# Kernel optimization log

Hardware: AMD Instinct MI355X
Metric: run time of the kernel (lower is better)

The kernel has to match this reference:

```python
import jax, jax.numpy as jnp
import numpy as np

N_NODES = 1024
H = 256        # hidden_dim
HEADS = 4
EPS = 1e-5     # torch LayerNorm default


def _ln(x, g, b):
    m = x.mean(-1, keepdims=True)
    v = ((x - m) ** 2).mean(-1, keepdims=True)
    return (x - m) / jnp.sqrt(v + EPS) * g + b


def setup_inputs() -> dict:
    key = jax.random.key(0)
    ks = jax.random.split(key, 24)
    B, L = 16, 64
    P = N_NODES * (N_NODES - 1) // 2
    D0 = L + 7  # latent_dim + 7 stats
    s = 0.02
    f32 = jnp.float32
    d = {}
    d['x'] = jax.random.normal(ks[0], (B, L), f32)
    d['stats'] = jax.random.normal(ks[1], (B, 7), f32)
    d['u'] = jax.random.uniform(ks[2], (B, P, 2), f32)  # uniform noise -> gumbel
    d['ln0_g'] = jnp.ones((D0,), f32); d['ln0_b'] = jnp.zeros((D0,), f32)
    # residual block 1 (in D0 -> H, has projection)
    d['rb1_ln_g'] = jnp.ones((D0,), f32); d['rb1_ln_b'] = jnp.zeros((D0,), f32)
    d['rb1_w1'] = jax.random.normal(ks[3], (H, D0), f32) * s; d['rb1_b1'] = jnp.zeros((H,), f32)
    d['rb1_w2'] = jax.random.normal(ks[4], (H, H), f32) * s;  d['rb1_b2'] = jnp.zeros((H,), f32)
    d['rb1_wp'] = jax.random.normal(ks[5], (H, D0), f32) * s; d['rb1_bp'] = jnp.zeros((H,), f32)
    # residual block 2 (H -> H, no projection)
    d['rb2_ln_g'] = jnp.ones((H,), f32); d['rb2_ln_b'] = jnp.zeros((H,), f32)
    d['rb2_w1'] = jax.random.normal(ks[6], (H, H), f32) * s; d['rb2_b1'] = jnp.zeros((H,), f32)
    d['rb2_w2'] = jax.random.normal(ks[7], (H, H), f32) * s; d['rb2_b2'] = jnp.zeros((H,), f32)
    # GraphAttention: LN + MHA(in_proj, out_proj) + output Linear
    d['att_ln_g'] = jnp.ones((H,), f32); d['att_ln_b'] = jnp.zeros((H,), f32)
    d['att_win'] = jax.random.normal(ks[8], (3 * H, H), f32) * s; d['att_bin'] = jnp.zeros((3 * H,), f32)
    d['att_wout'] = jax.random.normal(ks[9], (H, H), f32) * s;    d['att_bout'] = jnp.zeros((H,), f32)
    d['out_w'] = jax.random.normal(ks[10], (H, H), f32) * s;      d['out_b'] = jnp.zeros((H,), f32)
    # final edge-logit layer over concat([h_i, h_j]) -> 2
    d['fin_w'] = jax.random.normal(ks[11], (2, 2 * H), f32) * s;  d['fin_b'] = jnp.zeros((2,), f32)
    d['temp'] = jnp.ones((1,), f32)
    return d


def reference(x, stats, u, ln0_g, ln0_b,
              rb1_ln_g, rb1_ln_b, rb1_w1, rb1_b1, rb1_w2, rb1_b2, rb1_wp, rb1_bp,
              rb2_ln_g, rb2_ln_b, rb2_w1, rb2_b1, rb2_w2, rb2_b2,
              att_ln_g, att_ln_b, att_win, att_bin, att_wout, att_bout,
              out_w, out_b, fin_w, fin_b, temp):
    B = x.shape[0]
    z = jnp.concatenate([x, stats], axis=-1)          # [B, D0]
    z = _ln(z, ln0_g, ln0_b)
    h = jnp.broadcast_to(z[:, None, :], (B, N_NODES, z.shape[-1]))  # [B, N, D0]
    # residual block 1 (dropout in eval mode = identity)
    t = _ln(h, rb1_ln_g, rb1_ln_b)
    t = jax.nn.gelu(t @ rb1_w1.T + rb1_b1, approximate=False)
    t = t @ rb1_w2.T + rb1_b2
    h = t + (h @ rb1_wp.T + rb1_bp)                   # [B, N, H]
    # residual block 2
    t = _ln(h, rb2_ln_g, rb2_ln_b)
    t = jax.nn.gelu(t @ rb2_w1.T + rb2_b1, approximate=False)
    t = t @ rb2_w2.T + rb2_b2
    h = t + h
    # GraphAttention: LN -> self MHA -> output linear
    a = _ln(h, att_ln_g, att_ln_b)
    qkv = a @ att_win.T + att_bin                      # [B, N, 3H]
    q, k, v = jnp.split(qkv, 3, axis=-1)
    dh = H // HEADS
    def heads(t):
        return t.reshape(B, N_NODES, HEADS, dh).transpose(0, 2, 1, 3)
    q, k, v = heads(q), heads(k), heads(v)
    scores = jnp.einsum('bhqd,bhkd->bhqk', q, k) * np.float32(1.0 / np.sqrt(dh))
    att = jax.nn.softmax(scores, axis=-1)
    o = jnp.einsum('bhqk,bhkd->bhqd', att, v).transpose(0, 2, 1, 3).reshape(B, N_NODES, H)
    o = o @ att_wout.T + att_bout
    h = o @ out_w.T + out_b                            # [B, N, H]
    # pairwise edge logits: Linear(cat(h_i, h_j)) == h_i @ W_a^T + h_j @ W_b^T + b
    la = h @ fin_w[:, :H].T                            # [B, N, 2]
    lb = h @ fin_w[:, H:].T                            # [B, N, 2]
    iu, ju = jnp.triu_indices(N_NODES, k=1)
    logits = la[:, iu] + lb[:, ju] + fin_b             # [B, P, 2]
    # gumbel-softmax (hard, straight-through), tau = |temperature|
    tau = jnp.abs(temp)[0]
    g = -jnp.log(-jnp.log(u + 1e-10) + 1e-10)
    y_soft = jax.nn.softmax((logits + g) / tau, axis=-1)
    y_hard = jax.nn.one_hot(jnp.argmax(y_soft, axis=-1), 2, dtype=y_soft.dtype)
    y = y_hard + y_soft - jax.lax.stop_gradient(y_soft)
    e = y[..., 0]                                      # [B, P]
    adj = jnp.zeros((B, N_NODES, N_NODES), e.dtype).at[:, iu, ju].set(e)
    return adj + adj.transpose(0, 2, 1)
```

## Files before the change

kernel.cpp:

```cpp
#include <hip/hip_runtime.h>
#include <math.h>


#define NN    1024
#define HD    256
#define DIN0  71
#define NPAIR 523776
#define TILE  64
#define NT    16

__device__ __forceinline__ double blk_reduce(double v, double* red) {
  const int t = threadIdx.x;
  red[t] = v;
  __syncthreads();
  #pragma unroll
  for (int s = 128; s > 0; s >>= 1) {
    if (t < s) red[t] += red[t + s];
    __syncthreads();
  }
  double r = red[0];
  __syncthreads();
  return r;
}

__device__ __forceinline__ void ln_to(const double* src, double* dst, int D,
                                      const float* __restrict__ gam,
                                      const float* __restrict__ bet,
                                      double* red) {
  const int tid = threadIdx.x;
  double v = (tid < D) ? src[tid] : 0.0;
  double m = blk_reduce(v, red) / (double)D;
  double d = (tid < D) ? (src[tid] - m) : 0.0;
  double var = blk_reduce(d * d, red) / (double)D;
  double inv = 1.0 / sqrt(var + (double)1e-5f);
  if (tid < D) dst[tid] = d * inv * (double)gam[tid] + (double)bet[tid];
  __syncthreads();
}

__device__ __forceinline__ double dotw(const double* src, int Din,
                                       const float* __restrict__ W, int row) {
  const float* wr = W + (size_t)row * Din;
  double acc = 0.0;
  if ((Din & 3) == 0) {
    const float4* w4 = reinterpret_cast<const float4*>(wr);
    const int n4 = Din >> 2;
    #pragma unroll 4
    for (int i = 0; i < n4; ++i) {
      float4 w = w4[i];
      acc += src[4*i+0] * (double)w.x;
      acc += src[4*i+1] * (double)w.y;
      acc += src[4*i+2] * (double)w.z;
      acc += src[4*i+3] * (double)w.w;
    }
  } else {
    for (int i = 0; i < Din; ++i) acc += src[i] * (double)wr[i];
  }
  return acc;
}

__device__ __forceinline__ double gelu_exact(double x) {
  return 0.5 * x * (1.0 + erf(x * 0.70710678118654752440));
}

__global__ __launch_bounds__(256)
void head_kernel(const float* __restrict__ x, const float* __restrict__ stats,
                 const float* __restrict__ ln0_g, const float* __restrict__ ln0_b,
                 const float* __restrict__ rb1_ln_g, const float* __restrict__ rb1_ln_b,
                 const float* __restrict__ rb1_w1, const float* __restrict__ rb1_b1,
                 const float* __restrict__ rb1_w2, const float* __restrict__ rb1_b2,
                 const float* __restrict__ rb1_wp, const float* __restrict__ rb1_bp,
                 const float* __restrict__ rb2_ln_g, const float* __restrict__ rb2_ln_b,
                 const float* __restrict__ rb2_w1, const float* __restrict__ rb2_b1,
                 const float* __restrict__ rb2_w2, const float* __restrict__ rb2_b2,
                 const float* __restrict__ att_ln_g, const float* __restrict__ att_ln_b,
                 const float* __restrict__ att_win, const float* __restrict__ att_bin,
                 const float* __restrict__ att_wout, const float* __restrict__ att_bout,
                 const float* __restrict__ out_w, const float* __restrict__ out_b,
                 const float* __restrict__ fin_w, const float* __restrict__ fin_b,
                 double* __restrict__ c_out) {
  __shared__ double h[HD], t[HD], g[HD], red[256];
  const int tid = threadIdx.x;
  const int b = blockIdx.x;

  if (tid < DIN0)
    h[tid] = (tid < 64) ? (double)x[b * 64 + tid] : (double)stats[b * 7 + tid - 64];
  __syncthreads();

  ln_to(h, h, DIN0, ln0_g, ln0_b, red);

  ln_to(h, t, DIN0, rb1_ln_g, rb1_ln_b, red);
  g[tid] = gelu_exact(dotw(t, DIN0, rb1_w1, tid) + (double)rb1_b1[tid]);
  __syncthreads();
  {
    double t2 = dotw(g, HD, rb1_w2, tid) + (double)rb1_b2[tid];
    double pr = dotw(h, DIN0, rb1_wp, tid) + (double)rb1_bp[tid];
    __syncthreads();
    h[tid] = t2 + pr;
  }
  __syncthreads();

  ln_to(h, t, HD, rb2_ln_g, rb2_ln_b, red);
  g[tid] = gelu_exact(dotw(t, HD, rb2_w1, tid) + (double)rb2_b1[tid]);
  __syncthreads();
  {
    double t2 = dotw(g, HD, rb2_w2, tid) + (double)rb2_b2[tid];
    h[tid] = h[tid] + t2;
  }
  __syncthreads();

  ln_to(h, t, HD, att_ln_g, att_ln_b, red);
  g[tid] = dotw(t, HD, att_win + 2 * HD * HD, tid) + (double)att_bin[2 * HD + tid];
  __syncthreads();
  t[tid] = dotw(g, HD, att_wout, tid) + (double)att_bout[tid];
  __syncthreads();
  double hj = dotw(t, HD, out_w, tid) + (double)out_b[tid];

  double v0 = hj * (double)fin_w[tid]          + hj * (double)fin_w[HD + tid];
  double v1 = hj * (double)fin_w[2 * HD + tid] + hj * (double)fin_w[3 * HD + tid];
  double c0 = blk_reduce(v0, red) + (double)fin_b[0];
  double c1 = blk_reduce(v1, red) + (double)fin_b[1];
  if (tid == 0) {
    c_out[2 * b + 0] = c0;
    c_out[2 * b + 1] = c1;
  }
}

__global__ __launch_bounds__(256)
void adj_tile_kernel(const float* __restrict__ u, const double* __restrict__ c,
                     float* __restrict__ out) {
  __shared__ float tile[TILE][TILE + 1];
  const int b = blockIdx.y;
  int k = blockIdx.x;
  int ti = 0;
  while (k >= NT - ti) { k -= NT - ti; ++ti; }
  const int tj = ti + k;
  const bool diag = (ti == tj);

  const int t        = threadIdx.x;
  const int lane_col = (t & 15) << 2;
  const int row_base = t >> 4;
  const double c0 = c[2 * b + 0];
  const double c1 = c[2 * b + 1];
  const float* ub = u + (size_t)b * (2u * NPAIR);
  float* ob = out + ((size_t)b << 20);

  #pragma unroll
  for (int s = 0; s < 4; ++s) {
    const int il = s * 16 + row_base;
    const int i  = ti * TILE + il;
    const int rb = i * (2 * NN - 1 - i) / 2 - i - 1;
    float4 ev4;
    float* ev = &ev4.x;
    #pragma unroll
    for (int q = 0; q < 4; ++q) {
      const int jl = lane_col + q;
      const int j  = tj * TILE + jl;
      float e = 0.0f;
      if (j > i) {
        const int p = rb + j;
        const float2 uu = *reinterpret_cast<const float2*>(ub + 2 * p);
        const float g0 = -logf(-logf(uu.x + 1e-10f) + 1e-10f);
        const float g1 = -logf(-logf(uu.y + 1e-10f) + 1e-10f);
        e = ((c0 + (double)g0) >= (c1 + (double)g1)) ? 1.0f : 0.0f;
      }
      ev[q] = e;
      tile[il][jl] = e;
    }
    if (!diag) {
      *reinterpret_cast<float4*>(ob + (size_t)i * NN + tj * TILE + lane_col) = ev4;
    }
  }
  __syncthreads();

  #pragma unroll
  for (int s = 0; s < 4; ++s) {
    const int rl = s * 16 + row_base;
    if (!diag) {
      float4 v = make_float4(tile[lane_col + 0][rl], tile[lane_col + 1][rl],
                             tile[lane_col + 2][rl], tile[lane_col + 3][rl]);
      *reinterpret_cast<float4*>(ob + (size_t)(tj * TILE + rl) * NN
                                    + ti * TILE + lane_col) = v;
    } else {
      float v[4];
      #pragma unroll
      for (int q = 0; q < 4; ++q) {
        const int jl = lane_col + q;
        v[q] = (jl > rl) ? tile[rl][jl] : ((jl < rl) ? tile[jl][rl] : 0.0f);
      }
      *reinterpret_cast<float4*>(ob + (size_t)(ti * TILE + rl) * NN
                                    + ti * TILE + lane_col)
          = make_float4(v[0], v[1], v[2], v[3]);
    }
  }
}

extern "C" void kernel_launch(void* const* d_in, const int* in_sizes, int n_in,
                              void* d_out, int out_size, void* d_ws, size_t ws_size,
                              hipStream_t stream) {
  const float* x        = (const float*)d_in[0];
  const float* stats    = (const float*)d_in[1];
  const float* u        = (const float*)d_in[2];
  const float* ln0_g    = (const float*)d_in[3];
  const float* ln0_b    = (const float*)d_in[4];
  const float* rb1_ln_g = (const float*)d_in[5];
  const float* rb1_ln_b = (const float*)d_in[6];
  const float* rb1_w1   = (const float*)d_in[7];
  const float* rb1_b1   = (const float*)d_in[8];
  const float* rb1_w2   = (const float*)d_in[9];
  const float* rb1_b2   = (const float*)d_in[10];
  const float* rb1_wp   = (const float*)d_in[11];
  const float* rb1_bp   = (const float*)d_in[12];
  const float* rb2_ln_g = (const float*)d_in[13];
  const float* rb2_ln_b = (const float*)d_in[14];
  const float* rb2_w1   = (const float*)d_in[15];
  const float* rb2_b1   = (const float*)d_in[16];
  const float* rb2_w2   = (const float*)d_in[17];
  const float* rb2_b2   = (const float*)d_in[18];
  const float* att_ln_g = (const float*)d_in[19];
  const float* att_ln_b = (const float*)d_in[20];
  const float* att_win  = (const float*)d_in[21];
  const float* att_bin  = (const float*)d_in[22];
  const float* att_wout = (const float*)d_in[23];
  const float* att_bout = (const float*)d_in[24];
  const float* out_w    = (const float*)d_in[25];
  const float* out_b    = (const float*)d_in[26];
  const float* fin_w    = (const float*)d_in[27];
  const float* fin_b    = (const float*)d_in[28];

  double* c_ws = (double*)d_ws;
  float* out   = (float*)d_out;

  hipLaunchKernelGGL(head_kernel, dim3(16), dim3(256), 0, stream,
                     x, stats, ln0_g, ln0_b,
                     rb1_ln_g, rb1_ln_b, rb1_w1, rb1_b1, rb1_w2, rb1_b2, rb1_wp, rb1_bp,
                     rb2_ln_g, rb2_ln_b, rb2_w1, rb2_b1, rb2_w2, rb2_b2,
                     att_ln_g, att_ln_b, att_win, att_bin, att_wout, att_bout,
                     out_w, out_b, fin_w, fin_b, c_ws);

  hipLaunchKernelGGL(adj_tile_kernel, dim3(NT * (NT + 1) / 2, 16), dim3(256), 0, stream,
                     u, c_ws, out);
}
```

Before: 252.0 us.

## Prefetch weights into cache, use wave-shuffle reductions and split dot accumulators

A separate kernel launches before the head kernel and reads all MLP and attention weight matrices, so they are cache-resident when the 16-block head kernel streams them. Eight blocks per stripe read the same data, apparently so every L2 slice is warmed. The shared-memory tree reduction is replaced by a 64-lane shuffle plus a four-wave combine, which cuts the number of barriers. The float4 dot product now uses four independent double accumulators to shorten the dependency chain. The extra launch and redundant reads add overhead, and the summation order changes slightly.

```diff
diff --git a/kernel.cpp b/kernel.cpp
--- a/kernel.cpp
+++ b/kernel.cpp
@@ -9,18 +9,50 @@
 #define TILE  64
 #define NT    16
 
+__device__ __forceinline__ float pf_sum(const float4* __restrict__ p, int n4,
+                                        int stripe, int tid) {
+  float s = 0.0f;
+  for (int i = stripe * 256 + tid; i < n4; i += 256 * 256) {
+    float4 v = p[i];
+    s += v.x + v.y + v.z + v.w;
+  }
+  return s;
+}
+
+__global__ __launch_bounds__(256)
+void prefetch_kernel(const float* __restrict__ w0, int n0,
+                     const float* __restrict__ w1, int n1,
+                     const float* __restrict__ w2, int n2,
+                     const float* __restrict__ w3, int n3,
+                     const float* __restrict__ w4, int n4_,
+                     const float* __restrict__ w5, int n5,
+                     const float* __restrict__ w6, int n6,
+                     const float* __restrict__ w7, int n7,
+                     const float* __restrict__ w8, int n8,
+                     float* __restrict__ sink) {
+  const int stripe = blockIdx.x >> 3;
+  const int tid = threadIdx.x;
+  float s = 0.0f;
+  s += pf_sum((const float4*)w0, n0 >> 2, stripe, tid);
+  s += pf_sum((const float4*)w1, n1 >> 2, stripe, tid);
+  s += pf_sum((const float4*)w2, n2 >> 2, stripe, tid);
+  s += pf_sum((const float4*)w3, n3 >> 2, stripe, tid);
+  s += pf_sum((const float4*)w4, n4_ >> 2, stripe, tid);
+  s += pf_sum((const float4*)w5, n5 >> 2, stripe, tid);
+  s += pf_sum((const float4*)w6, n6 >> 2, stripe, tid);
+  s += pf_sum((const float4*)w7, n7 >> 2, stripe, tid);
+  s += pf_sum((const float4*)w8, n8 >> 2, stripe, tid);
+  if (s == 123456789.0f) sink[0] = s;
+}
+
 __device__ __forceinline__ double blk_reduce(double v, double* red) {
-  const int t = threadIdx.x;
-  red[t] = v;
-  __syncthreads();
   #pragma unroll
-  for (int s = 128; s > 0; s >>= 1) {
-    if (t < s) red[t] += red[t + s];
-    __syncthreads();
-  }
-  double r = red[0];
-  __syncthreads();
-  return r;
+  for (int m = 32; m > 0; m >>= 1) v += __shfl_xor(v, m, 64);
+  const int wid = threadIdx.x >> 6;
+  __syncthreads();
+  if ((threadIdx.x & 63) == 0) red[wid] = v;
+  __syncthreads();
+  return (red[0] + red[1]) + (red[2] + red[3]);
 }
 
 __device__ __forceinline__ void ln_to(const double* src, double* dst, int D,
@@ -40,21 +72,22 @@
 __device__ __forceinline__ double dotw(const double* src, int Din,
                                        const float* __restrict__ W, int row) {
   const float* wr = W + (size_t)row * Din;
-  double acc = 0.0;
   if ((Din & 3) == 0) {
     const float4* w4 = reinterpret_cast<const float4*>(wr);
     const int n4 = Din >> 2;
+    double a0 = 0.0, a1 = 0.0, a2 = 0.0, a3 = 0.0;
     #pragma unroll 4
     for (int i = 0; i < n4; ++i) {
       float4 w = w4[i];
-      acc += src[4*i+0] * (double)w.x;
-      acc += src[4*i+1] * (double)w.y;
-      acc += src[4*i+2] * (double)w.z;
-      acc += src[4*i+3] * (double)w.w;
-    }
-  } else {
-    for (int i = 0; i < Din; ++i) acc += src[i] * (double)wr[i];
-  }
+      a0 += src[4*i+0] * (double)w.x;
+      a1 += src[4*i+1] * (double)w.y;
+      a2 += src[4*i+2] * (double)w.z;
+      a3 += src[4*i+3] * (double)w.w;
+    }
+    return (a0 + a1) + (a2 + a3);
+  }
+  double acc = 0.0;
+  for (int i = 0; i < Din; ++i) acc += src[i] * (double)wr[i];
   return acc;
 }
 
@@ -78,7 +111,7 @@
                  const float* __restrict__ out_w, const float* __restrict__ out_b,
                  const float* __restrict__ fin_w, const float* __restrict__ fin_b,
                  double* __restrict__ c_out) {
-  __shared__ double h[HD], t[HD], g[HD], red[256];
+  __shared__ double h[HD], t[HD], g[HD], red[8];
   const int tid = threadIdx.x;
   const int b = blockIdx.x;
 
@@ -228,7 +261,20 @@
   const float* fin_b    = (const float*)d_in[28];
 
   double* c_ws = (double*)d_ws;
+  float* sink  = (float*)d_ws + 64;
   float* out   = (float*)d_out;
+
+  hipLaunchKernelGGL(prefetch_kernel, dim3(2048), dim3(256), 0, stream,
+                     rb1_w1, HD * DIN0 - (HD * DIN0 % 4),
+                     rb1_w2, HD * HD,
+                     rb1_wp, HD * DIN0 - (HD * DIN0 % 4),
+                     rb2_w1, HD * HD,
+                     rb2_w2, HD * HD,
+                     att_win + 2 * HD * HD, HD * HD,
+                     att_wout, HD * HD,
+                     out_w, HD * HD,
+                     fin_w, 4 * HD,
+                     sink);
 
   hipLaunchKernelGGL(head_kernel, dim3(16), dim3(256), 0, stream,
                      x, stats, ln0_g, ln0_b,
```

After: 248.0 us. Within noise of the previous version (-1.6%).

## Split head MLP dot products across four threads per row with shuffle reductions

Applied to the files above, without the earlier changes.

The head kernel now runs 1024 threads per block, and each output row's dot product is split across a quad of four threads whose partial sums are combined with xor shuffles. The shared-memory tree block reduction is replaced by a wavefront shuffle reduction followed by a small cross-wave sum. The goal is to shorten the serial, latency-bound per-batch head stage that runs on only 16 blocks. The cost is a larger block and more barriers of 1024 threads, and the head stage may be a small share of total time next to the adjacency kernel.

```diff
diff --git a/kernel.cpp b/kernel.cpp
--- a/kernel.cpp
+++ b/kernel.cpp
@@ -8,19 +8,19 @@
 #define NPAIR 523776
 #define TILE  64
 #define NT    16
+#define HT    1024
 
 __device__ __forceinline__ double blk_reduce(double v, double* red) {
-  const int t = threadIdx.x;
-  red[t] = v;
-  __syncthreads();
-  #pragma unroll
-  for (int s = 128; s > 0; s >>= 1) {
-    if (t < s) red[t] += red[t + s];
-    __syncthreads();
-  }
-  double r = red[0];
-  __syncthreads();
-  return r;
+  #pragma unroll
+  for (int m = 32; m > 0; m >>= 1) v += __shfl_xor(v, m, 64);
+  const int wid = threadIdx.x >> 6;
+  __syncthreads();
+  if ((threadIdx.x & 63) == 0) red[wid] = v;
+  __syncthreads();
+  double s = 0.0;
+  #pragma unroll
+  for (int w = 0; w < HT / 64; ++w) s += red[w];
+  return s;
 }
 
 __device__ __forceinline__ void ln_to(const double* src, double* dst, int D,
@@ -37,32 +37,45 @@
   __syncthreads();
 }
 
-__device__ __forceinline__ double dotw(const double* src, int Din,
-                                       const float* __restrict__ W, int row) {
-  const float* wr = W + (size_t)row * Din;
-  double acc = 0.0;
-  if ((Din & 3) == 0) {
-    const float4* w4 = reinterpret_cast<const float4*>(wr);
-    const int n4 = Din >> 2;
-    #pragma unroll 4
-    for (int i = 0; i < n4; ++i) {
-      float4 w = w4[i];
-      acc += src[4*i+0] * (double)w.x;
-      acc += src[4*i+1] * (double)w.y;
-      acc += src[4*i+2] * (double)w.z;
-      acc += src[4*i+3] * (double)w.w;
-    }
-  } else {
-    for (int i = 0; i < Din; ++i) acc += src[i] * (double)wr[i];
-  }
-  return acc;
+__device__ __forceinline__ double dot4_256(const double* src,
+                                           const float* __restrict__ W,
+                                           int row, int p) {
+  const float4* w4 = reinterpret_cast<const float4*>(W + (size_t)row * 256);
+  double a0 = 0.0, a1 = 0.0, a2 = 0.0, a3 = 0.0;
+  #pragma unroll
+  for (int k = 0; k < 16; ++k) {
+    const int f = p + 4 * k;
+    float4 w = w4[f];
+    const double* s = src + 4 * f;
+    a0 += s[0] * (double)w.x;
+    a1 += s[1] * (double)w.y;
+    a2 += s[2] * (double)w.z;
+    a3 += s[3] * (double)w.w;
+  }
+  return (a0 + a1) + (a2 + a3);
+}
+
+__device__ __forceinline__ double dot4_71(const double* src,
+                                          const float* __restrict__ W,
+                                          int row, int p) {
+  const float* wr = W + (size_t)row * DIN0;
+  double a = 0.0;
+  #pragma unroll
+  for (int i = p; i < DIN0; i += 4) a += src[i] * (double)wr[i];
+  return a;
+}
+
+__device__ __forceinline__ double quad_sum(double v) {
+  v += __shfl_xor(v, 1, 64);
+  v += __shfl_xor(v, 2, 64);
+  return v;
 }
 
 __device__ __forceinline__ double gelu_exact(double x) {
   return 0.5 * x * (1.0 + erf(x * 0.70710678118654752440));
 }
 
-__global__ __launch_bounds__(256)
+__global__ __launch_bounds__(HT)
 void head_kernel(const float* __restrict__ x, const float* __restrict__ stats,
                  const float* __restrict__ ln0_g, const float* __restrict__ ln0_b,
                  const float* __restrict__ rb1_ln_g, const float* __restrict__ rb1_ln_b,
@@ -78,9 +91,11 @@
                  const float* __restrict__ out_w, const float* __restrict__ out_b,
                  const float* __restrict__ fin_w, const float* __restrict__ fin_b,
                  double* __restrict__ c_out) {
-  __shared__ double h[HD], t[HD], g[HD], red[256];
+  __shared__ double h[HD], t[HD], g[HD], red[HT / 64];
   const int tid = threadIdx.x;
   const int b = blockIdx.x;
+  const int r = tid >> 2;
+  const int p = tid & 3;
 
   if (tid < DIN0)
     h[tid] = (tid < 64) ? (double)x[b * 64 + tid] : (double)stats[b * 7 + tid - 64];
@@ -89,34 +104,54 @@
   ln_to(h, h, DIN0, ln0_g, ln0_b, red);
 
   ln_to(h, t, DIN0, rb1_ln_g, rb1_ln_b, red);
-  g[tid] = gelu_exact(dotw(t, DIN0, rb1_w1, tid) + (double)rb1_b1[tid]);
-  __syncthreads();
-  {
-    double t2 = dotw(g, HD, rb1_w2, tid) + (double)rb1_b2[tid];
-    double pr = dotw(h, DIN0, rb1_wp, tid) + (double)rb1_bp[tid];
+  {
+    double d = quad_sum(dot4_71(t, rb1_w1, r, p));
+    if (p == 0) g[r] = gelu_exact(d + (double)rb1_b1[r]);
+  }
+  __syncthreads();
+  {
+    double d2 = quad_sum(dot4_256(g, rb1_w2, r, p));
+    double dp = quad_sum(dot4_71(h, rb1_wp, r, p));
     __syncthreads();
-    h[tid] = t2 + pr;
+    if (p == 0) h[r] = (d2 + (double)rb1_b2[r]) + (dp + (double)rb1_bp[r]);
   }
   __syncthreads();
 
   ln_to(h, t, HD, rb2_ln_g, rb2_ln_b, red);
-  g[tid] = gelu_exact(dotw(t, HD, rb2_w1, tid) + (double)rb2_b1[tid]);
-  __syncthreads();
-  {
-    double t2 = dotw(g, HD, rb2_w2, tid) + (double)rb2_b2[tid];
-    h[tid] = h[tid] + t2;
+  {
+    double d = quad_sum(dot4_256(t, rb2_w1, r, p));
+    if (p == 0) g[r] = gelu_exact(d + (double)rb2_b1[r]);
+  }
+  __syncthreads();
+  {
+    double d = quad_sum(dot4_256(g, rb2_w2, r, p));
+    if (p == 0) h[r] = h[r] + (d + (double)rb2_b2[r]);
   }
   __syncthreads();
 
   ln_to(h, t, HD, att_ln_g, att_ln_b, red);
-  g[tid] = dotw(t, HD, att_win + 2 * HD * HD, tid) + (double)att_bin[2 * HD + tid];
-  __syncthreads();
-  t[tid] = dotw(g, HD, att_wout, tid) + (double)att_bout[tid];
-  __syncthreads();
-  double hj = dotw(t, HD, out_w, tid) + (double)out_b[tid];
-
-  double v0 = hj * (double)fin_w[tid]          + hj * (double)fin_w[HD + tid];
-  double v1 = hj * (double)fin_w[2 * HD + tid] + hj * (double)fin_w[3 * HD + tid];
+  {
+    double d = quad_sum(dot4_256(t, att_win + 2 * HD * HD, r, p));
+    if (p == 0) g[r] = d + (double)att_bin[2 * HD + r];
+  }
+  __syncthreads();
+  {
+    double d = quad_sum(dot4_256(g, att_wout, r, p));
+    if (p == 0) t[r] = d + (double)att_bout[r];
+  }
+  __syncthreads();
+  {
+    double d = quad_sum(dot4_256(t, out_w, r, p));
+    if (p == 0) g[r] = d + (double)out_b[r];
+  }
+  __syncthreads();
+
+  double v0 = 0.0, v1 = 0.0;
+  if (tid < HD) {
+    const double hj = g[tid];
+    v0 = hj * (double)fin_w[tid]          + hj * (double)fin_w[HD + tid];
+    v1 = hj * (double)fin_w[2 * HD + tid] + hj * (double)fin_w[3 * HD + tid];
+  }
   double c0 = blk_reduce(v0, red) + (double)fin_b[0];
   double c1 = blk_reduce(v1, red) + (double)fin_b[1];
   if (tid == 0) {
@@ -157,8 +192,8 @@
       const int j  = tj * TILE + jl;
       float e = 0.0f;
       if (j > i) {
-        const int p = rb + j;
-        const float2 uu = *reinterpret_cast<const float2*>(ub + 2 * p);
+        const int p2 = rb + j;
+        const float2 uu = *reinterpret_cast<const float2*>(ub + 2 * p2);
         const float g0 = -logf(-logf(uu.x + 1e-10f) + 1e-10f);
         const float g1 = -logf(-logf(uu.y + 1e-10f) + 1e-10f);
         e = ((c0 + (double)g0) >= (c1 + (double)g1)) ? 1.0f : 0.0f;
@@ -230,7 +265,7 @@
   double* c_ws = (double*)d_ws;
   float* out   = (float*)d_out;
 
-  hipLaunchKernelGGL(head_kernel, dim3(16), dim3(256), 0, stream,
+  hipLaunchKernelGGL(head_kernel, dim3(16), dim3(HT), 0, stream,
                      x, stats, ln0_g, ln0_b,
                      rb1_ln_g, rb1_ln_b, rb1_w1, rb1_b1, rb1_w2, rb1_b2, rb1_wp, rb1_bp,
                      rb2_ln_g, rb2_ln_b, rb2_w1, rb2_b1, rb2_w2, rb2_b2,
```

Result: faster. 236.4 us (-6.2%).
